# Performance work log

Measured on AMD Instinct MI355X. Metric: run time of the kernel, lower is better.

## Reference

```python
import jax, jax.numpy as jnp
import numpy as np
from jax import lax

WIN = 9  # window size per spatial dim


def setup_inputs() -> dict:
    key = jax.random.key(0)
    k1, k2 = jax.random.split(key)
    shape = (2, 1, 160, 192, 160)  # [B, C=1, D, H, W]
    y_true = jax.random.uniform(k1, shape, dtype=jnp.float32)
    y_pred = jax.random.uniform(k2, shape, dtype=jnp.float32)
    return {"y_true": y_true, "y_pred": y_pred}


def reference(y_true, y_pred):
    Ii, Ji = y_true, y_pred
    ndims = Ii.ndim - 2  # 3 for volumes
    pad = WIN // 2
    # all five maps in the channel dim: [B, 5, D, H, W]
    all_five = jnp.concatenate([Ii, Ji, Ii * Ii, Ji * Ji, Ii * Ji], axis=1)
    # grouped box-filter conv: ones kernel [O=5, I/g=1, 9,9,9]
    kernel = jnp.ones((5, 1) + (WIN,) * ndims, dtype=Ii.dtype)
    conv = lax.conv_general_dilated(
        all_five, kernel,
        window_strides=(1,) * ndims,
        padding=[(pad, pad)] * ndims,
        feature_group_count=5,
        dimension_numbers=("NCDHW", "OIDHW", "NCDHW"),
    )
    I_sum, J_sum, I2_sum, J2_sum, IJ_sum = jnp.split(conv, 5, axis=1)
    win_size = jnp.asarray(float(WIN), dtype=Ii.dtype)
    cross = IJ_sum - J_sum / win_size * I_sum
    I_var = I2_sum - I_sum / win_size * I_sum
    J_var = J2_sum - J_sum / win_size * J_sum
    cc = cross * cross / (I_var * J_var + 1e-5)
    return -jnp.mean(cc)
```

## Files before the change

### kernel.cpp

```cpp
#include <hip/hip_runtime.h>

#define B_ 2
#define D_ 160
#define H_ 192
#define W_ 160
#define W4_ (W_ / 4)
#define HW_ (H_ * W_)
#define DHW_ (D_ * HW_)
#define NV_ ((long long)B_ * D_ * H_ * W_)

#define XT 32
#define NXT (W_ / XT)
#define YCH1 6
#define NYC1 (H_ / YCH1)
#define SPAD 4

#define ROWS2 8
#define ZCH2 10
#define NZC2 (D_ / ZCH2)
#define PAD 4
#define LROW (W_ + 2 * PAD)

#define SLAB ((size_t)H_ * 5 * XT)
#define A_Z  ((size_t)NXT * SLAB)

typedef _Float16 half4 __attribute__((ext_vector_type(4)));

__global__ void k_zero(double* acc) { *acc = 0.0; }

__device__ __forceinline__ void add4h(float4& d, const half4 v) {
    d.x += (float)v.x; d.y += (float)v.y; d.z += (float)v.z; d.w += (float)v.w;
}
__device__ __forceinline__ void sub4h(float4& d, const half4 v) {
    d.x -= (float)v.x; d.y -= (float)v.y; d.z -= (float)v.z; d.w -= (float)v.w;
}

template<int SGN>
__device__ __forceinline__ void acc_lds(float4 s[5], const half4 ha, const half4 hb) {
    const float4 a = make_float4((float)ha.x, (float)ha.y, (float)ha.z, (float)ha.w);
    const float4 b = make_float4((float)hb.x, (float)hb.y, (float)hb.z, (float)hb.w);
    if (SGN > 0) {
        s[0].x += a.x;     s[0].y += a.y;     s[0].z += a.z;     s[0].w += a.w;
        s[1].x += b.x;     s[1].y += b.y;     s[1].z += b.z;     s[1].w += b.w;
        s[2].x += a.x*a.x; s[2].y += a.y*a.y; s[2].z += a.z*a.z; s[2].w += a.w*a.w;
        s[3].x += b.x*b.x; s[3].y += b.y*b.y; s[3].z += b.z*b.z; s[3].w += b.w*b.w;
        s[4].x += a.x*b.x; s[4].y += a.y*b.y; s[4].z += a.z*b.z; s[4].w += a.w*b.w;
    } else {
        s[0].x -= a.x;     s[0].y -= a.y;     s[0].z -= a.z;     s[0].w -= a.w;
        s[1].x -= b.x;     s[1].y -= b.y;     s[1].z -= b.z;     s[1].w -= b.w;
        s[2].x -= a.x*a.x; s[2].y -= a.y*a.y; s[2].z -= a.z*a.z; s[2].w -= a.w*a.w;
        s[3].x -= b.x*b.x; s[3].y -= b.y*b.y; s[3].z -= b.z*b.z; s[3].w -= b.w*b.w;
        s[4].x -= a.x*b.x; s[4].y -= a.y*b.y; s[4].z -= a.z*b.z; s[4].w -= a.w*b.w;
    }
}

__global__ __launch_bounds__(256) void k1_ysum(const float* __restrict__ I,
                                               const float* __restrict__ J,
                                               _Float16* __restrict__ A) {
    __shared__ _Float16 sI[H_][XT + SPAD];
    __shared__ _Float16 sJ[H_][XT + SPAD];
    const int tid = threadIdx.x;
    const int xt  = blockIdx.x % NXT;
    const int bz  = blockIdx.x / NXT;
    const int x0  = xt * XT;

    const float* Ibase = I + (size_t)bz * HW_ + x0;
    const float* Jbase = J + (size_t)bz * HW_ + x0;

#pragma unroll
    for (int i = 0; i < 6; ++i) {
        const int idx = i * 256 + tid;
        const int row = idx >> 3;
        const int g   = idx & 7;
        const float4 vi = *(const float4*)(Ibase + (size_t)row * W_ + g * 4);
        const float4 vj = *(const float4*)(Jbase + (size_t)row * W_ + g * 4);
        half4 hi, hj;
        hi.x = (_Float16)vi.x; hi.y = (_Float16)vi.y; hi.z = (_Float16)vi.z; hi.w = (_Float16)vi.w;
        hj.x = (_Float16)vj.x; hj.y = (_Float16)vj.y; hj.z = (_Float16)vj.z; hj.w = (_Float16)vj.w;
        *(half4*)&sI[row][g * 4] = hi;
        *(half4*)&sJ[row][g * 4] = hj;
    }
    __syncthreads();

    const int xg = tid & 7;
    const int yc = tid >> 3;
    const int y0 = yc * YCH1;
    const int x4 = xg * 4;

    _Float16* Ap = A + ((size_t)bz * NXT + xt) * SLAB + x4;

    float4 s[5];
#pragma unroll
    for (int c = 0; c < 5; ++c) s[c] = make_float4(0, 0, 0, 0);

#pragma unroll
    for (int j = 0; j < 8; ++j) {
        const int yin = y0 - 4 + j;
        if (yin >= 0)
            acc_lds<+1>(s, *(const half4*)&sI[yin][x4], *(const half4*)&sJ[yin][x4]);
    }
#pragma unroll
    for (int k = 0; k < YCH1; ++k) {
        const int yi = y0 + k + 4;
        if (yi < H_)
            acc_lds<+1>(s, *(const half4*)&sI[yi][x4], *(const half4*)&sJ[yi][x4]);
        const int yo = y0 + k - 5;
        if (yo >= 0)
            acc_lds<-1>(s, *(const half4*)&sI[yo][x4], *(const half4*)&sJ[yo][x4]);

        _Float16* Ay = Ap + (size_t)(y0 + k) * (5 * XT);
#pragma unroll
        for (int c = 0; c < 5; ++c) {
            half4 h;
            h.x = (_Float16)s[c].x; h.y = (_Float16)s[c].y;
            h.z = (_Float16)s[c].z; h.w = (_Float16)s[c].w;
            *(half4*)(Ay + c * XT) = h;
        }
    }
}

__global__ void k2_zxcc(const _Float16* __restrict__ A, double* __restrict__ acc) {
    __shared__ float sbuf[ROWS2][5][LROW];
    __shared__ float red[512];
    const int tid = threadIdx.x;
    const int r   = tid / W4_;
    const int l   = tid - r * W4_;
    const int x4  = l * 4;
    const int xt  = l >> 3;
    const int xl4 = (l & 7) * 4;
    const int blk = blockIdx.x;
    const int zc  = blk % NZC2;
    const int rp  = blk / NZC2;
    const int gy  = rp * ROWS2 + r;
    const int b   = gy / H_;
    const int yy  = gy - b * H_;
    const int z0  = zc * ZCH2;

    {
        float* p = &sbuf[0][0][0];
        for (int i = tid; i < ROWS2 * 5 * LROW; i += ROWS2 * W4_) p[i] = 0.f;
    }

    const _Float16* Abase = A + ((size_t)b * D_) * A_Z + (size_t)xt * SLAB
                              + (size_t)yy * (5 * XT) + xl4;

    float4 s[5];
#pragma unroll
    for (int c = 0; c < 5; ++c) s[c] = make_float4(0, 0, 0, 0);
#pragma unroll
    for (int j = 0; j < 8; ++j) {
        const int zi = z0 - 4 + j;
        if (zi >= 0) {
            const _Float16* Az = Abase + (size_t)zi * A_Z;
#pragma unroll
            for (int c = 0; c < 5; ++c)
                add4h(s[c], *(const half4*)(Az + c * XT));
        }
    }
    __syncthreads();

    float local = 0.f;
    for (int k = 0; k < ZCH2; ++k) {
        const int zi = z0 + k + 4;
        if (zi < D_) {
            const _Float16* Az = Abase + (size_t)zi * A_Z;
#pragma unroll
            for (int c = 0; c < 5; ++c)
                add4h(s[c], *(const half4*)(Az + c * XT));
        }
        const int zo = z0 + k - 5;
        if (zo >= 0) {
            const _Float16* Az = Abase + (size_t)zo * A_Z;
#pragma unroll
            for (int c = 0; c < 5; ++c)
                sub4h(s[c], *(const half4*)(Az + c * XT));
        }
#pragma unroll
        for (int c = 0; c < 5; ++c)
            *(float4*)&sbuf[r][c][PAD + x4] = s[c];
        __syncthreads();

        float4 S5[5];
#pragma unroll
        for (int c = 0; c < 5; ++c) {
            const float4 a0 = *(const float4*)&sbuf[r][c][x4];
            const float4 a1 = *(const float4*)&sbuf[r][c][x4 + 4];
            const float4 a2 = *(const float4*)&sbuf[r][c][x4 + 8];
            const float o0 = a0.x + a0.y + a0.z + a0.w + a1.x + a1.y + a1.z + a1.w + a2.x;
            const float o1 = o0 - a0.x + a2.y;
            const float o2 = o1 - a0.y + a2.z;
            const float o3 = o2 - a0.z + a2.w;
            S5[c] = make_float4(o0, o1, o2, o3);
        }
        const float inv9 = 1.0f / 9.0f;
        {
            const float cr = S5[4].x - S5[1].x * S5[0].x * inv9;
            const float iv = S5[2].x - S5[0].x * S5[0].x * inv9;
            const float jv = S5[3].x - S5[1].x * S5[1].x * inv9;
            local += cr * cr / (iv * jv + 1e-5f);
        }
        {
            const float cr = S5[4].y - S5[1].y * S5[0].y * inv9;
            const float iv = S5[2].y - S5[0].y * S5[0].y * inv9;
            const float jv = S5[3].y - S5[1].y * S5[1].y * inv9;
            local += cr * cr / (iv * jv + 1e-5f);
        }
        {
            const float cr = S5[4].z - S5[1].z * S5[0].z * inv9;
            const float iv = S5[2].z - S5[0].z * S5[0].z * inv9;
            const float jv = S5[3].z - S5[1].z * S5[1].z * inv9;
            local += cr * cr / (iv * jv + 1e-5f);
        }
        {
            const float cr = S5[4].w - S5[1].w * S5[0].w * inv9;
            const float iv = S5[2].w - S5[0].w * S5[0].w * inv9;
            const float jv = S5[3].w - S5[1].w * S5[1].w * inv9;
            local += cr * cr / (iv * jv + 1e-5f);
        }
        __syncthreads();
    }

    red[tid] = local;
    if (tid < 192) red[320 + tid] = 0.f;
    __syncthreads();
    for (int off = 256; off > 0; off >>= 1) {
        if (tid < off) red[tid] += red[tid + off];
        __syncthreads();
    }
    if (tid == 0) atomicAdd(acc, (double)red[0]);
}

__global__ void p_direct(const float* __restrict__ I, const float* __restrict__ J,
                         double* __restrict__ acc) {
    const long long idx = (long long)blockIdx.x * blockDim.x + threadIdx.x;
    float local = 0.f;
    if (idx < NV_) {
        const int x = (int)(idx % W_);
        long long t = idx / W_;
        const int y = (int)(t % H_);
        t /= H_;
        const int z = (int)(t % D_);
        const int b = (int)(t / D_);
        const int z0 = max(z - 4, 0), z1 = min(z + 4, D_ - 1);
        const int y0 = max(y - 4, 0), y1 = min(y + 4, H_ - 1);
        const int x0 = max(x - 4, 0), x1 = min(x + 4, W_ - 1);
        float sI = 0.f, sJ = 0.f, sI2 = 0.f, sJ2 = 0.f, sIJ = 0.f;
        for (int zz = z0; zz <= z1; ++zz)
            for (int yy = y0; yy <= y1; ++yy) {
                const size_t row = ((size_t)(b * D_ + zz) * H_ + yy) * W_;
                for (int xx = x0; xx <= x1; ++xx) {
                    const float a = I[row + xx];
                    const float bb = J[row + xx];
                    sI += a; sJ += bb; sI2 += a * a; sJ2 += bb * bb; sIJ += a * bb;
                }
            }
        const float inv9 = 1.0f / 9.0f;
        const float cross = sIJ - sJ * sI * inv9;
        const float iv    = sI2 - sI * sI * inv9;
        const float jv    = sJ2 - sJ * sJ * inv9;
        local = cross * cross / (iv * jv + 1e-5f);
    }
    __shared__ float red[256];
    red[threadIdx.x] = local;
    __syncthreads();
    for (int off = 128; off > 0; off >>= 1) {
        if (threadIdx.x < off) red[threadIdx.x] += red[threadIdx.x + off];
        __syncthreads();
    }
    if (threadIdx.x == 0) atomicAdd(acc, (double)red[0]);
}

__global__ void k_final(const double* __restrict__ acc, float* __restrict__ out) {
    out[0] = (float)(-(*acc) / (double)NV_);
}

extern "C" void kernel_launch(void* const* d_in, const int* in_sizes, int n_in,
                              void* d_out, int out_size, void* d_ws, size_t ws_size,
                              hipStream_t stream) {
    const float* I = (const float*)d_in[0];
    const float* J = (const float*)d_in[1];
    float* out = (float*)d_out;

    const size_t needA = (size_t)5 * B_ * DHW_ * sizeof(_Float16);
    if (ws_size >= 1024 + needA) {
        double* acc = (double*)d_ws;
        _Float16* A = (_Float16*)((char*)d_ws + 1024);
        k_zero<<<1, 1, 0, stream>>>(acc);
        k1_ysum<<<B_ * D_ * NXT, 256, 0, stream>>>(I, J, A);
        k2_zxcc<<<NZC2 * (B_ * H_ / ROWS2), ROWS2 * W4_, 0, stream>>>(A, acc);
        k_final<<<1, 1, 0, stream>>>(acc, out);
    } else if (ws_size >= sizeof(double)) {
        double* acc = (double*)d_ws;
        k_zero<<<1, 1, 0, stream>>>(acc);
        p_direct<<<(int)((NV_ + 255) / 256), 256, 0, stream>>>(I, J, acc);
        k_final<<<1, 1, 0, stream>>>(acc, out);
    }
}
```

Baseline: 80.88 us.

## Move x-direction box sum into first pass, make z pass LDS-free

The first kernel now loads a 4-column halo on each side of its 32-wide x tile. It keeps y-direction running sums for three adjacent float4 column groups and combines them into the 9-wide x box sum before writing the fp16 intermediate. The second kernel then only slides along z and evaluates the cross-correlation term in registers. That removes its shared-memory staging buffer and the two barriers per z step, and it uses longer z chunks with smaller blocks. In exchange the first pass does roughly three times the LDS reads and accumulation work, plus halo loads with boundary zero-fill.

```diff
diff --git a/kernel.cpp b/kernel.cpp
--- a/kernel.cpp
+++ b/kernel.cpp
@@ -4,30 +4,29 @@
 #define D_ 160
 #define H_ 192
 #define W_ 160
-#define W4_ (W_ / 4)
 #define HW_ (H_ * W_)
 #define DHW_ (D_ * HW_)
 #define NV_ ((long long)B_ * D_ * H_ * W_)
 
 #define XT 32
 #define NXT (W_ / XT)
+#define SCOLS 40
+#define SSTR 52
 #define YCH1 6
-#define NYC1 (H_ / YCH1)
-#define SPAD 4
-
-#define ROWS2 8
-#define ZCH2 10
-#define NZC2 (D_ / ZCH2)
-#define PAD 4
-#define LROW (W_ + 2 * PAD)
+
+#define ZCH3 16
+#define NZC3 (D_ / ZCH3)
 
 #define SLAB ((size_t)H_ * 5 * XT)
-#define A_Z  ((size_t)NXT * SLAB)
+#define A2_Z ((size_t)NXT * SLAB)
 
 typedef _Float16 half4 __attribute__((ext_vector_type(4)));
 
 __global__ void k_zero(double* acc) { *acc = 0.0; }
 
+__device__ __forceinline__ float4 h2f(const half4 h) {
+    return make_float4((float)h.x, (float)h.y, (float)h.z, (float)h.w);
+}
 __device__ __forceinline__ void add4h(float4& d, const half4 v) {
     d.x += (float)v.x; d.y += (float)v.y; d.z += (float)v.z; d.w += (float)v.w;
 }
@@ -36,194 +35,187 @@
 }
 
 template<int SGN>
-__device__ __forceinline__ void acc_lds(float4 s[5], const half4 ha, const half4 hb) {
-    const float4 a = make_float4((float)ha.x, (float)ha.y, (float)ha.z, (float)ha.w);
-    const float4 b = make_float4((float)hb.x, (float)hb.y, (float)hb.z, (float)hb.w);
+__device__ __forceinline__ void accP(float4 ys[3][5], int t, const float4 a, const float4 b) {
     if (SGN > 0) {
-        s[0].x += a.x;     s[0].y += a.y;     s[0].z += a.z;     s[0].w += a.w;
-        s[1].x += b.x;     s[1].y += b.y;     s[1].z += b.z;     s[1].w += b.w;
-        s[2].x += a.x*a.x; s[2].y += a.y*a.y; s[2].z += a.z*a.z; s[2].w += a.w*a.w;
-        s[3].x += b.x*b.x; s[3].y += b.y*b.y; s[3].z += b.z*b.z; s[3].w += b.w*b.w;
-        s[4].x += a.x*b.x; s[4].y += a.y*b.y; s[4].z += a.z*b.z; s[4].w += a.w*b.w;
+        ys[t][0].x += a.x;     ys[t][0].y += a.y;     ys[t][0].z += a.z;     ys[t][0].w += a.w;
+        ys[t][1].x += b.x;     ys[t][1].y += b.y;     ys[t][1].z += b.z;     ys[t][1].w += b.w;
+        ys[t][2].x += a.x*a.x; ys[t][2].y += a.y*a.y; ys[t][2].z += a.z*a.z; ys[t][2].w += a.w*a.w;
+        ys[t][3].x += b.x*b.x; ys[t][3].y += b.y*b.y; ys[t][3].z += b.z*b.z; ys[t][3].w += b.w*b.w;
+        ys[t][4].x += a.x*b.x; ys[t][4].y += a.y*b.y; ys[t][4].z += a.z*b.z; ys[t][4].w += a.w*b.w;
     } else {
-        s[0].x -= a.x;     s[0].y -= a.y;     s[0].z -= a.z;     s[0].w -= a.w;
-        s[1].x -= b.x;     s[1].y -= b.y;     s[1].z -= b.z;     s[1].w -= b.w;
-        s[2].x -= a.x*a.x; s[2].y -= a.y*a.y; s[2].z -= a.z*a.z; s[2].w -= a.w*a.w;
-        s[3].x -= b.x*b.x; s[3].y -= b.y*b.y; s[3].z -= b.z*b.z; s[3].w -= b.w*b.w;
-        s[4].x -= a.x*b.x; s[4].y -= a.y*b.y; s[4].z -= a.z*b.z; s[4].w -= a.w*b.w;
-    }
-}
-
-__global__ __launch_bounds__(256) void k1_ysum(const float* __restrict__ I,
-                                               const float* __restrict__ J,
-                                               _Float16* __restrict__ A) {
-    __shared__ _Float16 sI[H_][XT + SPAD];
-    __shared__ _Float16 sJ[H_][XT + SPAD];
+        ys[t][0].x -= a.x;     ys[t][0].y -= a.y;     ys[t][0].z -= a.z;     ys[t][0].w -= a.w;
+        ys[t][1].x -= b.x;     ys[t][1].y -= b.y;     ys[t][1].z -= b.z;     ys[t][1].w -= b.w;
+        ys[t][2].x -= a.x*a.x; ys[t][2].y -= a.y*a.y; ys[t][2].z -= a.z*a.z; ys[t][2].w -= a.w*a.w;
+        ys[t][3].x -= b.x*b.x; ys[t][3].y -= b.y*b.y; ys[t][3].z -= b.z*b.z; ys[t][3].w -= b.w*b.w;
+        ys[t][4].x -= a.x*b.x; ys[t][4].y -= a.y*b.y; ys[t][4].z -= a.z*b.z; ys[t][4].w -= a.w*b.w;
+    }
+}
+
+template<int SGN>
+__device__ __forceinline__ void accRow(float4 ys[3][5],
+                                       const _Float16* sIrow, const _Float16* sJrow,
+                                       int x4) {
+#pragma unroll
+    for (int t = 0; t < 3; ++t) {
+        const float4 a = h2f(*(const half4*)(sIrow + x4 + t * 4));
+        const float4 b = h2f(*(const half4*)(sJrow + x4 + t * 4));
+        accP<SGN>(ys, t, a, b);
+    }
+}
+
+__global__ __launch_bounds__(256) void k1_xysum(const float* __restrict__ I,
+                                                const float* __restrict__ J,
+                                                _Float16* __restrict__ A2) {
+    __shared__ _Float16 sI[H_][SSTR];
+    __shared__ _Float16 sJ[H_][SSTR];
     const int tid = threadIdx.x;
     const int xt  = blockIdx.x % NXT;
     const int bz  = blockIdx.x / NXT;
-    const int x0  = xt * XT;
-
-    const float* Ibase = I + (size_t)bz * HW_ + x0;
-    const float* Jbase = J + (size_t)bz * HW_ + x0;
-
-#pragma unroll
-    for (int i = 0; i < 6; ++i) {
+    const int xs0 = xt * XT - 4;
+
+    const float* Ib = I + (size_t)bz * HW_;
+    const float* Jb = J + (size_t)bz * HW_;
+
+#pragma unroll
+    for (int i = 0; i < 8; ++i) {
         const int idx = i * 256 + tid;
-        const int row = idx >> 3;
-        const int g   = idx & 7;
-        const float4 vi = *(const float4*)(Ibase + (size_t)row * W_ + g * 4);
-        const float4 vj = *(const float4*)(Jbase + (size_t)row * W_ + g * 4);
-        half4 hi, hj;
-        hi.x = (_Float16)vi.x; hi.y = (_Float16)vi.y; hi.z = (_Float16)vi.z; hi.w = (_Float16)vi.w;
-        hj.x = (_Float16)vj.x; hj.y = (_Float16)vj.y; hj.z = (_Float16)vj.z; hj.w = (_Float16)vj.w;
-        *(half4*)&sI[row][g * 4] = hi;
-        *(half4*)&sJ[row][g * 4] = hj;
+        if (idx < H_ * 10) {
+            const int row = idx / 10;
+            const int g   = idx - row * 10;
+            const int gx  = xs0 + g * 4;
+            half4 hi, hj;
+            hi.x = hi.y = hi.z = hi.w = (_Float16)0.f;
+            hj.x = hj.y = hj.z = hj.w = (_Float16)0.f;
+            if (gx >= 0 && gx + 3 < W_) {
+                const float4 vi = *(const float4*)(Ib + (size_t)row * W_ + gx);
+                const float4 vj = *(const float4*)(Jb + (size_t)row * W_ + gx);
+                hi.x = (_Float16)vi.x; hi.y = (_Float16)vi.y; hi.z = (_Float16)vi.z; hi.w = (_Float16)vi.w;
+                hj.x = (_Float16)vj.x; hj.y = (_Float16)vj.y; hj.z = (_Float16)vj.z; hj.w = (_Float16)vj.w;
+            }
+            *(half4*)&sI[row][g * 4] = hi;
+            *(half4*)&sJ[row][g * 4] = hj;
+        }
     }
     __syncthreads();
 
     const int xg = tid & 7;
     const int yc = tid >> 3;
+    const int x4 = xg * 4;
     const int y0 = yc * YCH1;
-    const int x4 = xg * 4;
-
-    _Float16* Ap = A + ((size_t)bz * NXT + xt) * SLAB + x4;
-
-    float4 s[5];
-#pragma unroll
-    for (int c = 0; c < 5; ++c) s[c] = make_float4(0, 0, 0, 0);
-
-#pragma unroll
-    for (int j = 0; j < 8; ++j) {
-        const int yin = y0 - 4 + j;
-        if (yin >= 0)
-            acc_lds<+1>(s, *(const half4*)&sI[yin][x4], *(const half4*)&sJ[yin][x4]);
-    }
+
+    _Float16* Ap = A2 + ((size_t)bz * NXT + xt) * SLAB + x4;
+
+    float4 ys[3][5];
+#pragma unroll
+    for (int t = 0; t < 3; ++t)
+#pragma unroll
+        for (int c = 0; c < 5; ++c) ys[t][c] = make_float4(0, 0, 0, 0);
+
+#pragma unroll
+    for (int j = 0; j < 9; ++j) {
+        const int yr = y0 - 5 + j;
+        if (yr >= 0) accRow<+1>(ys, &sI[yr][0], &sJ[yr][0], x4);
+    }
+
 #pragma unroll
     for (int k = 0; k < YCH1; ++k) {
         const int yi = y0 + k + 4;
-        if (yi < H_)
-            acc_lds<+1>(s, *(const half4*)&sI[yi][x4], *(const half4*)&sJ[yi][x4]);
+        if (yi < H_) accRow<+1>(ys, &sI[yi][0], &sJ[yi][0], x4);
         const int yo = y0 + k - 5;
-        if (yo >= 0)
-            acc_lds<-1>(s, *(const half4*)&sI[yo][x4], *(const half4*)&sJ[yo][x4]);
+        if (yo >= 0) accRow<-1>(ys, &sI[yo][0], &sJ[yo][0], x4);
 
         _Float16* Ay = Ap + (size_t)(y0 + k) * (5 * XT);
 #pragma unroll
         for (int c = 0; c < 5; ++c) {
+            const float4 u = ys[0][c], v = ys[1][c], w = ys[2][c];
+            const float o0 = u.x + u.y + u.z + u.w + v.x + v.y + v.z + v.w + w.x;
+            const float o1 = o0 - u.x + w.y;
+            const float o2 = o1 - u.y + w.z;
+            const float o3 = o2 - u.z + w.w;
             half4 h;
-            h.x = (_Float16)s[c].x; h.y = (_Float16)s[c].y;
-            h.z = (_Float16)s[c].z; h.w = (_Float16)s[c].w;
+            h.x = (_Float16)o0; h.y = (_Float16)o1; h.z = (_Float16)o2; h.w = (_Float16)o3;
             *(half4*)(Ay + c * XT) = h;
         }
     }
 }
 
-__global__ void k2_zxcc(const _Float16* __restrict__ A, double* __restrict__ acc) {
-    __shared__ float sbuf[ROWS2][5][LROW];
-    __shared__ float red[512];
+__global__ __launch_bounds__(256) void k2_zcc(const _Float16* __restrict__ A2,
+                                              double* __restrict__ acc) {
     const int tid = threadIdx.x;
-    const int r   = tid / W4_;
-    const int l   = tid - r * W4_;
-    const int x4  = l * 4;
-    const int xt  = l >> 3;
-    const int xl4 = (l & 7) * 4;
-    const int blk = blockIdx.x;
-    const int zc  = blk % NZC2;
-    const int rp  = blk / NZC2;
-    const int gy  = rp * ROWS2 + r;
-    const int b   = gy / H_;
-    const int yy  = gy - b * H_;
-    const int z0  = zc * ZCH2;
-
-    {
-        float* p = &sbuf[0][0][0];
-        for (int i = tid; i < ROWS2 * 5 * LROW; i += ROWS2 * W4_) p[i] = 0.f;
-    }
-
-    const _Float16* Abase = A + ((size_t)b * D_) * A_Z + (size_t)xt * SLAB
+    const int xl4 = (tid & 7) * 4;
+    const int yl  = tid >> 3;
+    int t = blockIdx.x;
+    const int zc   = t % NZC3;  t /= NZC3;
+    const int xt   = t % NXT;   t /= NXT;
+    const int ygrp = t;
+    const int gy   = ygrp * 32 + yl;
+    const int b    = gy / H_;
+    const int yy   = gy - b * H_;
+    const int z0   = zc * ZCH3;
+
+    const _Float16* base = A2 + (size_t)(b * D_) * A2_Z + (size_t)xt * SLAB
                               + (size_t)yy * (5 * XT) + xl4;
 
     float4 s[5];
 #pragma unroll
     for (int c = 0; c < 5; ++c) s[c] = make_float4(0, 0, 0, 0);
-#pragma unroll
-    for (int j = 0; j < 8; ++j) {
-        const int zi = z0 - 4 + j;
+
+#pragma unroll
+    for (int j = 0; j < 9; ++j) {
+        const int zi = z0 - 5 + j;
         if (zi >= 0) {
-            const _Float16* Az = Abase + (size_t)zi * A_Z;
-#pragma unroll
-            for (int c = 0; c < 5; ++c)
-                add4h(s[c], *(const half4*)(Az + c * XT));
-        }
-    }
-    __syncthreads();
+            const _Float16* p = base + (size_t)zi * A2_Z;
+#pragma unroll
+            for (int c = 0; c < 5; ++c) add4h(s[c], *(const half4*)(p + c * XT));
+        }
+    }
 
     float local = 0.f;
-    for (int k = 0; k < ZCH2; ++k) {
+    const float inv9 = 1.0f / 9.0f;
+#pragma unroll
+    for (int k = 0; k < ZCH3; ++k) {
         const int zi = z0 + k + 4;
         if (zi < D_) {
-            const _Float16* Az = Abase + (size_t)zi * A_Z;
-#pragma unroll
-            for (int c = 0; c < 5; ++c)
-                add4h(s[c], *(const half4*)(Az + c * XT));
+            const _Float16* p = base + (size_t)zi * A2_Z;
+#pragma unroll
+            for (int c = 0; c < 5; ++c) add4h(s[c], *(const half4*)(p + c * XT));
         }
         const int zo = z0 + k - 5;
         if (zo >= 0) {
-            const _Float16* Az = Abase + (size_t)zo * A_Z;
-#pragma unroll
-            for (int c = 0; c < 5; ++c)
-                sub4h(s[c], *(const half4*)(Az + c * XT));
-        }
-#pragma unroll
-        for (int c = 0; c < 5; ++c)
-            *(float4*)&sbuf[r][c][PAD + x4] = s[c];
-        __syncthreads();
-
-        float4 S5[5];
-#pragma unroll
-        for (int c = 0; c < 5; ++c) {
-            const float4 a0 = *(const float4*)&sbuf[r][c][x4];
-            const float4 a1 = *(const float4*)&sbuf[r][c][x4 + 4];
-            const float4 a2 = *(const float4*)&sbuf[r][c][x4 + 8];
-            const float o0 = a0.x + a0.y + a0.z + a0.w + a1.x + a1.y + a1.z + a1.w + a2.x;
-            const float o1 = o0 - a0.x + a2.y;
-            const float o2 = o1 - a0.y + a2.z;
-            const float o3 = o2 - a0.z + a2.w;
-            S5[c] = make_float4(o0, o1, o2, o3);
-        }
-        const float inv9 = 1.0f / 9.0f;
-        {
-            const float cr = S5[4].x - S5[1].x * S5[0].x * inv9;
-            const float iv = S5[2].x - S5[0].x * S5[0].x * inv9;
-            const float jv = S5[3].x - S5[1].x * S5[1].x * inv9;
-            local += cr * cr / (iv * jv + 1e-5f);
-        }
-        {
-            const float cr = S5[4].y - S5[1].y * S5[0].y * inv9;
-            const float iv = S5[2].y - S5[0].y * S5[0].y * inv9;
-            const float jv = S5[3].y - S5[1].y * S5[1].y * inv9;
-            local += cr * cr / (iv * jv + 1e-5f);
-        }
-        {
-            const float cr = S5[4].z - S5[1].z * S5[0].z * inv9;
-            const float iv = S5[2].z - S5[0].z * S5[0].z * inv9;
-            const float jv = S5[3].z - S5[1].z * S5[1].z * inv9;
-            local += cr * cr / (iv * jv + 1e-5f);
-        }
-        {
-            const float cr = S5[4].w - S5[1].w * S5[0].w * inv9;
-            const float iv = S5[2].w - S5[0].w * S5[0].w * inv9;
-            const float jv = S5[3].w - S5[1].w * S5[1].w * inv9;
-            local += cr * cr / (iv * jv + 1e-5f);
-        }
-        __syncthreads();
-    }
-
+            const _Float16* p = base + (size_t)zo * A2_Z;
+#pragma unroll
+            for (int c = 0; c < 5; ++c) sub4h(s[c], *(const half4*)(p + c * XT));
+        }
+        {
+            const float cr = s[4].x - s[1].x * s[0].x * inv9;
+            const float iv = s[2].x - s[0].x * s[0].x * inv9;
+            const float jv = s[3].x - s[1].x * s[1].x * inv9;
+            local += cr * cr / (iv * jv + 1e-5f);
+        }
+        {
+            const float cr = s[4].y - s[1].y * s[0].y * inv9;
+            const float iv = s[2].y - s[0].y * s[0].y * inv9;
+            const float jv = s[3].y - s[1].y * s[1].y * inv9;
+            local += cr * cr / (iv * jv + 1e-5f);
+        }
+        {
+            const float cr = s[4].z - s[1].z * s[0].z * inv9;
+            const float iv = s[2].z - s[0].z * s[0].z * inv9;
+            const float jv = s[3].z - s[1].z * s[1].z * inv9;
+            local += cr * cr / (iv * jv + 1e-5f);
+        }
+        {
+            const float cr = s[4].w - s[1].w * s[0].w * inv9;
+            const float iv = s[2].w - s[0].w * s[0].w * inv9;
+            const float jv = s[3].w - s[1].w * s[1].w * inv9;
+            local += cr * cr / (iv * jv + 1e-5f);
+        }
+    }
+
+    __shared__ float red[256];
     red[tid] = local;
-    if (tid < 192) red[320 + tid] = 0.f;
     __syncthreads();
-    for (int off = 256; off > 0; off >>= 1) {
+    for (int off = 128; off > 0; off >>= 1) {
         if (tid < off) red[tid] += red[tid + off];
         __syncthreads();
     }
@@ -284,10 +276,10 @@
     const size_t needA = (size_t)5 * B_ * DHW_ * sizeof(_Float16);
     if (ws_size >= 1024 + needA) {
         double* acc = (double*)d_ws;
-        _Float16* A = (_Float16*)((char*)d_ws + 1024);
+        _Float16* A2 = (_Float16*)((char*)d_ws + 1024);
         k_zero<<<1, 1, 0, stream>>>(acc);
-        k1_ysum<<<B_ * D_ * NXT, 256, 0, stream>>>(I, J, A);
-        k2_zxcc<<<NZC2 * (B_ * H_ / ROWS2), ROWS2 * W4_, 0, stream>>>(A, acc);
+        k1_xysum<<<B_ * D_ * NXT, 256, 0, stream>>>(I, J, A2);
+        k2_zcc<<<NZC3 * NXT * (B_ * H_ / 32), 256, 0, stream>>>(A2, acc);
         k_final<<<1, 1, 0, stream>>>(acc, out);
     } else if (ws_size >= sizeof(double)) {
         double* acc = (double*)d_ws;
```

Measured after the change: 136.7 us. 69.1% more time.
